# Performance work log

Hardware: AMD Instinct MI355X
Metric: run time of the kernel (lower is better)

The kernel has to match this reference:

```python
import jax, jax.numpy as jnp
import numpy as np

N_NODES = 50000
N_EDGES = 800000
N_GRAPHS = 64


def graph_conv(x, edge_index, w_rel, b_rel, w_root):
    # PyG GraphConv with aggr='add':
    #   out = lin_rel(sum_{j in N(i)} x_j) + lin_root(x_i)
    src, dst = edge_index[0], edge_index[1]
    agg = jax.ops.segment_sum(x[src], dst, num_segments=x.shape[0])  # [N, d_in]
    return agg @ w_rel + b_rel + x @ w_root  # [N, d_out]


def scatter_mean(x, batch, num_segments):
    s = jax.ops.segment_sum(x, batch, num_segments=num_segments)
    cnt = jax.ops.segment_sum(jnp.ones((x.shape[0],), x.dtype), batch,
                              num_segments=num_segments)
    return s / jnp.maximum(cnt, 1.0)[:, None]


def setup_inputs() -> dict:
    key = jax.random.key(0)
    ks = jax.random.split(key, 8)
    d_feat, d_hid, d_out = 128, 128, 128
    x = jax.random.normal(ks[0], (N_NODES, d_feat), dtype=jnp.float32)
    edge_index = jax.random.randint(ks[1], (2, N_EDGES), 0, N_NODES, dtype=jnp.int64)
    batch = jnp.sort(jax.random.randint(ks[2], (N_NODES,), 0, N_GRAPHS, dtype=jnp.int64))

    def glorot(k, shape):
        fan_in = shape[0]
        return jax.random.normal(k, shape, dtype=jnp.float32) / np.sqrt(fan_in)

    return {
        "x": x,
        "edge_index": edge_index,
        "batch": batch,
        "w_rel1": glorot(ks[3], (d_feat, d_hid)),
        "b_rel1": jnp.zeros((d_hid,), jnp.float32),
        "w_root1": glorot(ks[4], (d_feat, d_hid)),
        "w_rel2": glorot(ks[5], (d_hid, 2 * d_hid)),
        "b_rel2": jnp.zeros((2 * d_hid,), jnp.float32),
        "w_root2": glorot(ks[6], (d_hid, 2 * d_hid)),
        "w_rel3": glorot(ks[7], (2 * d_hid, d_out)),
        "b_rel3": jnp.zeros((d_out,), jnp.float32),
        "w_root3": glorot(jax.random.fold_in(key, 99), (2 * d_hid, d_out)),
    }


def reference(x, edge_index, batch,
              w_rel1, b_rel1, w_root1,
              w_rel2, b_rel2, w_root2,
              w_rel3, b_rel3, w_root3):
    h = jax.nn.elu(graph_conv(x, edge_index, w_rel1, b_rel1, w_root1))
    h = jax.nn.elu(graph_conv(h, edge_index, w_rel2, b_rel2, w_root2))
    h = jax.nn.elu(graph_conv(h, edge_index, w_rel3, b_rel3, w_root3))
    return scatter_mean(h, batch, N_GRAPHS)  # [num_graphs, n_out]
```

## Files before the change

kernel.cpp:

```cpp
#include <hip/hip_runtime.h>
#include <math.h>

#define NN 50000
#define NNP 50048
#define NE 800000
#define NG 64
#define NBK 196
#define ECH 4082
#define TOTH (NBK * NBK)
#define NBH 151
#define SBLK 6890
#define SWORK (NN * 32 + 163840)
#define AGB 12500

typedef __attribute__((ext_vector_type(8))) __bf16 bf16x8;
typedef __attribute__((ext_vector_type(4))) float f32x4;

__device__ inline unsigned short f2bf(float f) {
    unsigned int u = __float_as_uint(f);
    u += 0x7fffu + ((u >> 16) & 1u);
    return (unsigned short)(u >> 16);
}
__device__ inline float bflo(unsigned int v) { return __uint_as_float(v << 16); }
__device__ inline float bfhi(unsigned int v) { return __uint_as_float(v & 0xffff0000u); }
__device__ inline float bfs(unsigned short v) { return __uint_as_float((unsigned int)v << 16); }

#define GLD_LDS16(g, l)                                                          \
    __builtin_amdgcn_global_load_lds(                                            \
        (const __attribute__((address_space(1))) unsigned int*)(g),              \
        (__attribute__((address_space(3))) unsigned int*)(l), 16, 0, 0)

__global__ __launch_bounds__(256) void front_k(const float* __restrict__ x,
                                               const float* __restrict__ wr1,
                                               const float* __restrict__ wo1,
                                               const float* __restrict__ wr2,
                                               const float* __restrict__ wo2,
                                               const float* __restrict__ wr3,
                                               const float* __restrict__ wo3,
                                               const int* __restrict__ edst,
                                               const int* __restrict__ batch,
                                               unsigned short* __restrict__ xb,
                                               unsigned short* __restrict__ W1T,
                                               unsigned short* __restrict__ W2T,
                                               unsigned short* __restrict__ W3T,
                                               int* __restrict__ H,
                                               int* __restrict__ bounds,
                                               float* __restrict__ outp) {
    const int b = blockIdx.x, t = threadIdx.x;
    if (b < SBLK) {
        int id = b * 256 + t;
        if (id < NN * 32) {
            float4 v = ((const float4*)x)[id];
            unsigned int p0 = ((unsigned int)f2bf(v.y) << 16) | f2bf(v.x);
            unsigned int p1 = ((unsigned int)f2bf(v.w) << 16) | f2bf(v.z);
            ((uint2*)xb)[id] = make_uint2(p0, p1);
            return;
        }
        int w = id - NN * 32;
        if (w < 32768) {
            int n = w >> 8, k = w & 255;
            W1T[w] = f2bf((k < 128) ? wr1[k * 128 + n] : wo1[(k - 128) * 128 + n]);
        } else if (w < 98304) {
            int j = w - 32768; int n = j >> 8, k = j & 255;
            W2T[j] = f2bf((k < 128) ? wr2[k * 256 + n] : wo2[(k - 128) * 256 + n]);
        } else if (w < 163840) {
            int j = w - 98304; int n = j >> 8, k = j & 255;
            W3T[j] = f2bf((n < 128) ? wr3[k * 128 + n] : wo3[k * 128 + (n - 128)]);
        }
        return;
    }
    if (b < SBLK + NBK) {
        __shared__ int h[NBK];
        int k = b - SBLK;
        if (t < NBK) h[t] = 0;
        __syncthreads();
        int e0 = k * ECH, e1 = min(NE, e0 + ECH);
        for (int e = e0 + t; e < e1; e += 256) atomicAdd(&h[edst[e] >> 8], 1);
        __syncthreads();
        if (t < NBK) H[t * NBK + k] = h[t];
        return;
    }
    if (t <= NG) {
        int g = t, lo = 0, hi = NN;
        while (lo < hi) { int mid = (lo + hi) >> 1; if (batch[mid] < g) lo = mid + 1; else hi = mid; }
        bounds[g] = lo;
    }
    for (int i = t; i < NG * 128; i += 256) outp[i] = 0.f;
}

__global__ __launch_bounds__(256) void hsum_k(const int* __restrict__ H,
                                              int* __restrict__ hb) {
    int i = blockIdx.x * 256 + threadIdx.x;
    int v = (i < TOTH) ? H[i] : 0;
    for (int off = 32; off; off >>= 1) v += __shfl_xor(v, off, 64);
    __shared__ int ws[4];
    if ((threadIdx.x & 63) == 0) ws[threadIdx.x >> 6] = v;
    __syncthreads();
    if (threadIdx.x == 0) hb[blockIdx.x] = ws[0] + ws[1] + ws[2] + ws[3];
}

__global__ __launch_bounds__(256) void happly_k(const int* __restrict__ H,
                                                const int* __restrict__ hb,
                                                int* __restrict__ S) {
    __shared__ int s[256], ws[4], choff;
    const int t = threadIdx.x, c = blockIdx.x;
    {
        int v = (t < c) ? hb[t] : 0;
        for (int off = 32; off; off >>= 1) v += __shfl_xor(v, off, 64);
        if ((t & 63) == 0) ws[t >> 6] = v;
        __syncthreads();
        if (t == 0) choff = ws[0] + ws[1] + ws[2] + ws[3];
        __syncthreads();
    }
    int i = c * 256 + t;
    int v = (i < TOTH) ? H[i] : 0;
    s[t] = v; __syncthreads();
    for (int off = 1; off < 256; off <<= 1) {
        int u = (t >= off) ? s[t - off] : 0;
        __syncthreads(); s[t] += u; __syncthreads();
    }
    if (i < TOTH) S[i] = choff + s[t] - v;
}

__global__ __launch_bounds__(256) void scatter_k(const int* __restrict__ src,
                                                 const int* __restrict__ dst,
                                                 const int* __restrict__ S,
                                                 int* __restrict__ tmp) {
    __shared__ int cur[NBK];
    int t = threadIdx.x, k = blockIdx.x;
    if (t < NBK) cur[t] = S[t * NBK + k];
    __syncthreads();
    int e0 = k * ECH, e1 = min(NE, e0 + ECH);
    for (int e = e0 + t; e < e1; e += 256) {
        int d = dst[e];
        int p = atomicAdd(&cur[d >> 8], 1);
        tmp[p] = ((d & 255) << 16) | src[e];
    }
}

__global__ __launch_bounds__(256) void csr_k(const int* __restrict__ tmp,
                                             const int* __restrict__ S,
                                             int* __restrict__ rowptr,
                                             int* __restrict__ colsrc) {
    __shared__ int hist[256], off[256], cur[256];
    int t = threadIdx.x, b = blockIdx.x;
    int base = S[b * NBK];
    int next = (b < NBK - 1) ? S[(b + 1) * NBK] : NE;
    int cntb = next - base;
    hist[t] = 0;
    __syncthreads();
    for (int i = t; i < cntb; i += 256) atomicAdd(&hist[tmp[base + i] >> 16], 1);
    __syncthreads();
    int v = hist[t];
    off[t] = v; __syncthreads();
    for (int o = 1; o < 256; o <<= 1) {
        int u = (t >= o) ? off[t - o] : 0;
        __syncthreads(); off[t] += u; __syncthreads();
    }
    int excl = off[t] - v;
    int node = b * 256 + t;
    if (node <= NN) rowptr[node] = base + excl;
    cur[t] = excl;
    __syncthreads();
    for (int i = t; i < cntb; i += 256) {
        int e = tmp[base + i];
        int p = atomicAdd(&cur[e >> 16], 1);
        colsrc[base + p] = e & 0xffff;
    }
}

__global__ __launch_bounds__(256) void aggs_k(const unsigned short* __restrict__ feat,
                                              const int* __restrict__ rowptr,
                                              const int* __restrict__ colsrc,
                                              unsigned short* __restrict__ outp) {
    const int slice = blockIdx.x & 3;
    const int gid = threadIdx.x >> 4;
    const int l16 = threadIdx.x & 15;
    const int node = (blockIdx.x >> 2) * 16 + gid;
    const int fo = slice * 32 + l16 * 2;
    const int beg = rowptr[node], end = rowptr[node + 1];
    float ax = 0.f, ay = 0.f;
    int e = beg;
    for (; e + 8 <= end; e += 8) {
        int c[8];
#pragma unroll
        for (int i = 0; i < 8; ++i) c[i] = colsrc[e + i];
        unsigned int v[8];
#pragma unroll
        for (int i = 0; i < 8; ++i)
            v[i] = *(const unsigned int*)&feat[(size_t)c[i] * 128 + fo];
#pragma unroll
        for (int i = 0; i < 8; ++i) { ax += bflo(v[i]); ay += bfhi(v[i]); }
    }
    for (; e < end; ++e) {
        unsigned int v = *(const unsigned int*)&feat[(size_t)colsrc[e] * 128 + fo];
        ax += bflo(v); ay += bfhi(v);
    }
    unsigned int p = ((unsigned int)f2bf(ay) << 16) | f2bf(ax);
    *(unsigned int*)&outp[(size_t)node * 128 + fo] = p;
}

__global__ __launch_bounds__(256) void aggfs_k(const unsigned short* __restrict__ y,
                                               const unsigned short* __restrict__ rr,
                                               const float* __restrict__ b3,
                                               const int* __restrict__ rowptr,
                                               const int* __restrict__ colsrc,
                                               unsigned short* __restrict__ outp) {
    const int slice = blockIdx.x & 3;
    const int gid = threadIdx.x >> 4;
    const int l16 = threadIdx.x & 15;
    const int node = (blockIdx.x >> 2) * 16 + gid;
    const int fo = slice * 32 + l16 * 2;
    const int beg = rowptr[node], end = rowptr[node + 1];
    float ax = 0.f, ay = 0.f;
    int e = beg;
    for (; e + 8 <= end; e += 8) {
        int c[8];
#pragma unroll
        for (int i = 0; i < 8; ++i) c[i] = colsrc[e + i];
        unsigned int v[8];
#pragma unroll
        for (int i = 0; i < 8; ++i)
            v[i] = *(const unsigned int*)&y[(size_t)c[i] * 128 + fo];
#pragma unroll
        for (int i = 0; i < 8; ++i) { ax += bflo(v[i]); ay += bfhi(v[i]); }
    }
    for (; e < end; ++e) {
        unsigned int v = *(const unsigned int*)&y[(size_t)colsrc[e] * 128 + fo];
        ax += bflo(v); ay += bfhi(v);
    }
    unsigned int rv = *(const unsigned int*)&rr[(size_t)node * 128 + fo];
    float2 bb = *(const float2*)&b3[fo];
    float vx = ax + bflo(rv) + bb.x;
    float vy = ay + bfhi(rv) + bb.y;
    vx = vx > 0.f ? vx : (__expf(vx) - 1.f);
    vy = vy > 0.f ? vy : (__expf(vy) - 1.f);
    unsigned int p = ((unsigned int)f2bf(vy) << 16) | f2bf(vx);
    *(unsigned int*)&outp[(size_t)node * 128 + fo] = p;
}

template <int MT, int KA, int N, bool TWO, bool BIAS, bool ELU>
__global__ __launch_bounds__(256) void gemm_k(const unsigned short* __restrict__ A1,
                                              const unsigned short* __restrict__ A2,
                                              const unsigned short* __restrict__ WT,
                                              const float* __restrict__ bias,
                                              unsigned short* __restrict__ Cout) {
    constexpr int KTOT = TWO ? 2 * KA : KA;
    constexpr int NSTEP = KTOT / 32;
    constexpr int MI = MT / 32;
    constexpr int LA = MT / 64;
    constexpr int LB = N / 64;
    __shared__ __attribute__((aligned(16))) unsigned short As[2][MT * 32];
    __shared__ __attribute__((aligned(16))) unsigned short Bs[2][N * 32];
    const int t = threadIdx.x;
    const int wv = t >> 6, lane = t & 63;
    const int qd = lane >> 4, l16 = lane & 15;
    const int m0 = blockIdx.x * MT;
    const int mh = (wv & 1) * (MT / 2), nh = (wv >> 1) * 64;
    const int srow = lane >> 2;
    const int skk  = (lane & 3) * 8;

    f32x4 acc[MI][4] = {};

    auto stage = [&](int k0, int buf) {
        const unsigned short* Abase = (TWO && k0 >= KA) ? (A2 + (k0 - KA)) : (A1 + k0);
#pragma unroll
        for (int i = 0; i < LA; ++i) {
            int chunk = wv * LA + i;
            const unsigned short* g = Abase + (size_t)(m0 + chunk * 16 + srow) * KA + skk;
            GLD_LDS16(g, &As[buf][chunk * 512]);
        }
        const unsigned short* Wbase = WT + k0;
#pragma unroll
        for (int i = 0; i < LB; ++i) {
            int chunk = wv * LB + i;
            const unsigned short* g = Wbase + (size_t)(chunk * 16 + srow) * KTOT + skk;
            GLD_LDS16(g, &Bs[buf][chunk * 512]);
        }
    };

    stage(0, 0);
    for (int s = 0; s < NSTEP; ++s) {
        const int cur = s & 1;
        if (s + 1 < NSTEP) {
            stage((s + 1) * 32, cur ^ 1);
            asm volatile("s_waitcnt vmcnt(%0)" :: "i"(LA + LB) : "memory");
        } else {
            asm volatile("s_waitcnt vmcnt(0)" ::: "memory");
        }
        __builtin_amdgcn_s_barrier();
        asm volatile("" ::: "memory");
        bf16x8 af[MI], bfr[4];
#pragma unroll
        for (int mi = 0; mi < MI; ++mi)
            af[mi] = *(const bf16x8*)&As[cur][(mh + mi * 16 + l16) * 32 + qd * 8];
#pragma unroll
        for (int ni = 0; ni < 4; ++ni)
            bfr[ni] = *(const bf16x8*)&Bs[cur][(nh + ni * 16 + l16) * 32 + qd * 8];
#pragma unroll
        for (int mi = 0; mi < MI; ++mi)
#pragma unroll
            for (int ni = 0; ni < 4; ++ni)
                acc[mi][ni] = __builtin_amdgcn_mfma_f32_16x16x32_bf16(
                    af[mi], bfr[ni], acc[mi][ni], 0, 0, 0);
        asm volatile("" ::: "memory");
        __builtin_amdgcn_s_barrier();
    }

#pragma unroll
    for (int mi = 0; mi < MI; ++mi)
#pragma unroll
        for (int ni = 0; ni < 4; ++ni)
#pragma unroll
            for (int r = 0; r < 4; ++r) {
                int mm = m0 + mh + mi * 16 + qd * 4 + r;
                if (mm < NN) {
                    int nn = nh + ni * 16 + l16;
                    float v = acc[mi][ni][r];
                    if (BIAS) v += bias[nn];
                    if (ELU) v = v > 0.f ? v : (__expf(v) - 1.f);
                    Cout[(size_t)mm * N + nn] = f2bf(v);
                }
            }
}

template <int KA, bool TWO, bool BIAS, bool ELU, bool SPLIT>
__global__ __launch_bounds__(256) void gemm256_k(const unsigned short* __restrict__ A1,
                                                 const unsigned short* __restrict__ A2,
                                                 const unsigned short* __restrict__ WT,
                                                 const float* __restrict__ bias,
                                                 unsigned short* __restrict__ Cout,
                                                 unsigned short* __restrict__ Cout2) {
    constexpr int KTOT = TWO ? 2 * KA : KA;
    constexpr int NSTEP = KTOT / 32;
    __shared__ __attribute__((aligned(16))) unsigned short As[2][64 * 32];
    __shared__ __attribute__((aligned(16))) unsigned short Bs[2][256 * 32];
    const int t = threadIdx.x;
    const int wv = t >> 6, lane = t & 63;
    const int qd = lane >> 4, l16 = lane & 15;
    const int m0 = blockIdx.x * 64;
    const int srow = lane >> 2;
    const int skk  = (lane & 3) * 8;

    f32x4 acc[4][4] = {};

    auto stage = [&](int k0, int buf) {
        const unsigned short* Abase = (TWO && k0 >= KA) ? (A2 + (k0 - KA)) : (A1 + k0);
        {
            const unsigned short* g = Abase + (size_t)(m0 + wv * 16 + srow) * KA + skk;
            GLD_LDS16(g, &As[buf][wv * 512]);
        }
        const unsigned short* Wbase = WT + k0;
#pragma unroll
        for (int i = 0; i < 4; ++i) {
            int chunk = wv * 4 + i;
            const unsigned short* g = Wbase + (size_t)(chunk * 16 + srow) * KTOT + skk;
            GLD_LDS16(g, &Bs[buf][chunk * 512]);
        }
    };

    stage(0, 0);
    for (int s = 0; s < NSTEP; ++s) {
        const int cur = s & 1;
        if (s + 1 < NSTEP) {
            stage((s + 1) * 32, cur ^ 1);
            asm volatile("s_waitcnt vmcnt(%0)" :: "i"(5) : "memory");
        } else {
            asm volatile("s_waitcnt vmcnt(0)" ::: "memory");
        }
        __builtin_amdgcn_s_barrier();
        asm volatile("" ::: "memory");
        bf16x8 af[4], bfr[4];
#pragma unroll
        for (int mi = 0; mi < 4; ++mi)
            af[mi] = *(const bf16x8*)&As[cur][(mi * 16 + l16) * 32 + qd * 8];
#pragma unroll
        for (int ni = 0; ni < 4; ++ni)
            bfr[ni] = *(const bf16x8*)&Bs[cur][(wv * 64 + ni * 16 + l16) * 32 + qd * 8];
#pragma unroll
        for (int mi = 0; mi < 4; ++mi)
#pragma unroll
            for (int ni = 0; ni < 4; ++ni)
                acc[mi][ni] = __builtin_amdgcn_mfma_f32_16x16x32_bf16(
                    af[mi], bfr[ni], acc[mi][ni], 0, 0, 0);
        asm volatile("" ::: "memory");
        __builtin_amdgcn_s_barrier();
    }

#pragma unroll
    for (int mi = 0; mi < 4; ++mi)
#pragma unroll
        for (int ni = 0; ni < 4; ++ni)
#pragma unroll
            for (int r = 0; r < 4; ++r) {
                int mm = m0 + mi * 16 + qd * 4 + r;
                if (mm < NN) {
                    int nn = wv * 64 + ni * 16 + l16;
                    float v = acc[mi][ni][r];
                    if (BIAS) v += bias[nn];
                    if (ELU) v = v > 0.f ? v : (__expf(v) - 1.f);
                    unsigned short b = f2bf(v);
                    if (SPLIT) {
                        unsigned short* dst = (nn < 128) ? Cout : Cout2;
                        dst[(size_t)mm * 128 + (nn & 127)] = b;
                    } else {
                        Cout[(size_t)mm * 256 + nn] = b;
                    }
                }
            }
}

__global__ __launch_bounds__(256) void sum_k(const unsigned short* __restrict__ vals,
                                             const int* __restrict__ batch,
                                             float* __restrict__ outsum) {
    const int CH = 25;
    int wv = threadIdx.x >> 6, lane = threadIdx.x & 63;
    int n0 = (blockIdx.x * 4 + wv) * CH;
    int g = batch[n0];
    float ax = 0.f, ay = 0.f;
    for (int i = 0; i < CH; ++i) {
        int n = n0 + i;
        int gn = batch[n];
        if (gn != g) {
            unsafeAtomicAdd(&outsum[(size_t)g * 128 + lane * 2], ax);
            unsafeAtomicAdd(&outsum[(size_t)g * 128 + lane * 2 + 1], ay);
            ax = 0.f; ay = 0.f; g = gn;
        }
        unsigned int v = *(const unsigned int*)&vals[(size_t)n * 128 + lane * 2];
        ax += bflo(v); ay += bfhi(v);
    }
    unsafeAtomicAdd(&outsum[(size_t)g * 128 + lane * 2], ax);
    unsafeAtomicAdd(&outsum[(size_t)g * 128 + lane * 2 + 1], ay);
}

__global__ void divide_k(const int* __restrict__ bounds, float* __restrict__ out) {
    int i = blockIdx.x * 256 + threadIdx.x;
    if (i < NG * 128) {
        int g = i >> 7;
        float c = (float)(bounds[g + 1] - bounds[g]);
        out[i] /= fmaxf(c, 1.f);
    }
}

extern "C" void kernel_launch(void* const* d_in, const int* in_sizes, int n_in,
                              void* d_out, int out_size, void* d_ws, size_t ws_size,
                              hipStream_t stream) {
    const float* x       = (const float*)d_in[0];
    const int*   ei      = (const int*)d_in[1];
    const int*   batch   = (const int*)d_in[2];
    const float* w_rel1  = (const float*)d_in[3];
    const float* b_rel1  = (const float*)d_in[4];
    const float* w_root1 = (const float*)d_in[5];
    const float* w_rel2  = (const float*)d_in[6];
    const float* b_rel2  = (const float*)d_in[7];
    const float* w_root2 = (const float*)d_in[8];
    const float* w_rel3  = (const float*)d_in[9];
    const float* b_rel3  = (const float*)d_in[10];
    const float* w_root3 = (const float*)d_in[11];
    const int* esrc = ei;
    const int* edst = ei + NE;

    unsigned short* Ab = (unsigned short*)d_ws;
    unsigned short* Bb = Ab + (size_t)NNP * 128;
    unsigned short* Cb = Bb + (size_t)NNP * 128;
    unsigned short* xb = Cb + (size_t)NNP * 256;
    unsigned short* W1T = xb + (size_t)NNP * 128;
    unsigned short* W2T = W1T + 128 * 256;
    unsigned short* W3T = W2T + 256 * 256;
    int* rowptr = (int*)(W3T + 256 * 256);
    int* colsrc = rowptr + (NN + 1);
    int* tmp    = colsrc + NE;
    int* H      = tmp + NE;
    int* S      = H + TOTH;
    int* hb     = S + TOTH;
    int* bounds = hb + 256;
    float* outp = (float*)d_out;

    front_k<<<SBLK + NBK + 1, 256, 0, stream>>>(
        x, w_rel1, w_root1, w_rel2, w_root2, w_rel3, w_root3, edst, batch,
        xb, W1T, W2T, W3T, H, bounds, outp);
    hsum_k<<<NBH, 256, 0, stream>>>(H, hb);
    happly_k<<<NBH, 256, 0, stream>>>(H, hb, S);
    scatter_k<<<NBK, 256, 0, stream>>>(esrc, edst, S, tmp);
    csr_k<<<NBK, 256, 0, stream>>>(tmp, S, rowptr, colsrc);

    aggs_k<<<AGB, 256, 0, stream>>>(xb, rowptr, colsrc, Ab);
    gemm_k<64, 128, 128, true, true, true>
        <<<NNP / 64, 256, 0, stream>>>(Ab, xb, W1T, b_rel1, Bb);

    aggs_k<<<AGB, 256, 0, stream>>>(Bb, rowptr, colsrc, Ab);
    gemm256_k<128, true, true, true, false>
        <<<NNP / 64, 256, 0, stream>>>(Ab, Bb, W2T, b_rel2, Cb, nullptr);

    gemm256_k<256, false, false, false, true>
        <<<NNP / 64, 256, 0, stream>>>(Cb, nullptr, W3T, nullptr, Ab, Bb);

    aggfs_k<<<AGB, 256, 0, stream>>>(Ab, Bb, b_rel3, rowptr, colsrc, Cb);
    sum_k<<<NN / 100, 256, 0, stream>>>(Cb, batch, outp);
    divide_k<<<(NG * 128 + 255) / 256, 256, 0, stream>>>(bounds, outp);
}
```

Measured before the change: 362.9 us.

## Assign one wavefront per node in CSR aggregation with split edge halves

The three gather-aggregation kernels now map one 64-lane wavefront to each destination node instead of 16 lanes per node per 32-feature slice. Each half-wave handles alternate edges with 8-byte loads covering the full 128-feature row, and the halves are combined with a cross-lane shuffle before the bf16 store. This cuts redundant rowptr and colsrc reads, which were repeated by four slice blocks, and widens the per-lane loads. In exchange, half the lanes sit idle during the epilogue and store, and there is extra tail-handling code.

```diff
diff --git a/kernel.cpp b/kernel.cpp
--- a/kernel.cpp
+++ b/kernel.cpp
@@ -11,7 +11,6 @@
 #define NBH 151
 #define SBLK 6890
 #define SWORK (NN * 32 + 163840)
-#define AGB 12500
 
 typedef __attribute__((ext_vector_type(8))) __bf16 bf16x8;
 typedef __attribute__((ext_vector_type(4))) float f32x4;
@@ -169,74 +168,132 @@
     }
 }
 
-__global__ __launch_bounds__(256) void aggs_k(const unsigned short* __restrict__ feat,
+__global__ __launch_bounds__(256) void aggb_k(const unsigned short* __restrict__ feat,
                                               const int* __restrict__ rowptr,
                                               const int* __restrict__ colsrc,
                                               unsigned short* __restrict__ outp) {
-    const int slice = blockIdx.x & 3;
-    const int gid = threadIdx.x >> 4;
-    const int l16 = threadIdx.x & 15;
-    const int node = (blockIdx.x >> 2) * 16 + gid;
-    const int fo = slice * 32 + l16 * 2;
+    const int node = __builtin_amdgcn_readfirstlane((int)(blockIdx.x * 4 + (threadIdx.x >> 6)));
+    const int lane = threadIdx.x & 63;
+    const int half = lane >> 5, l32 = lane & 31;
     const int beg = rowptr[node], end = rowptr[node + 1];
-    float ax = 0.f, ay = 0.f;
+    float a0 = 0.f, a1 = 0.f, a2 = 0.f, a3 = 0.f;
     int e = beg;
-    for (; e + 8 <= end; e += 8) {
-        int c[8];
-#pragma unroll
-        for (int i = 0; i < 8; ++i) c[i] = colsrc[e + i];
-        unsigned int v[8];
+    for (; e + 16 <= end; e += 16) {
+        int c[8]; uint2 v[8];
+#pragma unroll
+        for (int i = 0; i < 8; ++i) c[i] = colsrc[e + 2 * i + half];
 #pragma unroll
         for (int i = 0; i < 8; ++i)
-            v[i] = *(const unsigned int*)&feat[(size_t)c[i] * 128 + fo];
-#pragma unroll
-        for (int i = 0; i < 8; ++i) { ax += bflo(v[i]); ay += bfhi(v[i]); }
-    }
-    for (; e < end; ++e) {
-        unsigned int v = *(const unsigned int*)&feat[(size_t)colsrc[e] * 128 + fo];
-        ax += bflo(v); ay += bfhi(v);
-    }
-    unsigned int p = ((unsigned int)f2bf(ay) << 16) | f2bf(ax);
-    *(unsigned int*)&outp[(size_t)node * 128 + fo] = p;
-}
-
-__global__ __launch_bounds__(256) void aggfs_k(const unsigned short* __restrict__ y,
-                                               const unsigned short* __restrict__ rr,
-                                               const float* __restrict__ b3,
-                                               const int* __restrict__ rowptr,
-                                               const int* __restrict__ colsrc,
-                                               unsigned short* __restrict__ outp) {
-    const int slice = blockIdx.x & 3;
-    const int gid = threadIdx.x >> 4;
-    const int l16 = threadIdx.x & 15;
-    const int node = (blockIdx.x >> 2) * 16 + gid;
-    const int fo = slice * 32 + l16 * 2;
+            v[i] = *(const uint2*)&feat[(size_t)c[i] * 128 + l32 * 4];
+#pragma unroll
+        for (int i = 0; i < 8; ++i) {
+            a0 += bflo(v[i].x); a1 += bfhi(v[i].x);
+            a2 += bflo(v[i].y); a3 += bfhi(v[i].y);
+        }
+    }
+    for (; e + 4 <= end; e += 4) {
+        int c[2]; uint2 v[2];
+#pragma unroll
+        for (int i = 0; i < 2; ++i) c[i] = colsrc[e + 2 * i + half];
+#pragma unroll
+        for (int i = 0; i < 2; ++i)
+            v[i] = *(const uint2*)&feat[(size_t)c[i] * 128 + l32 * 4];
+#pragma unroll
+        for (int i = 0; i < 2; ++i) {
+            a0 += bflo(v[i].x); a1 += bfhi(v[i].x);
+            a2 += bflo(v[i].y); a3 += bfhi(v[i].y);
+        }
+    }
+    if (e + 2 <= end) {
+        int c = colsrc[e + half];
+        uint2 v = *(const uint2*)&feat[(size_t)c * 128 + l32 * 4];
+        a0 += bflo(v.x); a1 += bfhi(v.x); a2 += bflo(v.y); a3 += bfhi(v.y);
+        e += 2;
+    }
+    if (e < end && half == 0) {
+        int c = colsrc[e];
+        uint2 v = *(const uint2*)&feat[(size_t)c * 128 + l32 * 4];
+        a0 += bflo(v.x); a1 += bfhi(v.x); a2 += bflo(v.y); a3 += bfhi(v.y);
+    }
+    a0 += __shfl_xor(a0, 32, 64);
+    a1 += __shfl_xor(a1, 32, 64);
+    a2 += __shfl_xor(a2, 32, 64);
+    a3 += __shfl_xor(a3, 32, 64);
+    if (half == 0) {
+        unsigned int p0 = ((unsigned int)f2bf(a1) << 16) | f2bf(a0);
+        unsigned int p1 = ((unsigned int)f2bf(a3) << 16) | f2bf(a2);
+        *(uint2*)&outp[(size_t)node * 128 + l32 * 4] = make_uint2(p0, p1);
+    }
+}
+
+__global__ __launch_bounds__(256) void aggf_k(const unsigned short* __restrict__ y,
+                                              const unsigned short* __restrict__ rr,
+                                              const float* __restrict__ b3,
+                                              const int* __restrict__ rowptr,
+                                              const int* __restrict__ colsrc,
+                                              unsigned short* __restrict__ outp) {
+    const int node = __builtin_amdgcn_readfirstlane((int)(blockIdx.x * 4 + (threadIdx.x >> 6)));
+    const int lane = threadIdx.x & 63;
+    const int half = lane >> 5, l32 = lane & 31;
     const int beg = rowptr[node], end = rowptr[node + 1];
-    float ax = 0.f, ay = 0.f;
+    float a0 = 0.f, a1 = 0.f, a2 = 0.f, a3 = 0.f;
     int e = beg;
-    for (; e + 8 <= end; e += 8) {
-        int c[8];
-#pragma unroll
-        for (int i = 0; i < 8; ++i) c[i] = colsrc[e + i];
-        unsigned int v[8];
+    for (; e + 16 <= end; e += 16) {
+        int c[8]; uint2 v[8];
+#pragma unroll
+        for (int i = 0; i < 8; ++i) c[i] = colsrc[e + 2 * i + half];
 #pragma unroll
         for (int i = 0; i < 8; ++i)
-            v[i] = *(const unsigned int*)&y[(size_t)c[i] * 128 + fo];
-#pragma unroll
-        for (int i = 0; i < 8; ++i) { ax += bflo(v[i]); ay += bfhi(v[i]); }
-    }
-    for (; e < end; ++e) {
-        unsigned int v = *(const unsigned int*)&y[(size_t)colsrc[e] * 128 + fo];
-        ax += bflo(v); ay += bfhi(v);
-    }
-    unsigned int rv = *(const unsigned int*)&rr[(size_t)node * 128 + fo];
-    float2 bb = *(const float2*)&b3[fo];
-    float vx = ax + bflo(rv) + bb.x;
-    float vy = ay + bfhi(rv) + bb.y;
-    vx = vx > 0.f ? vx : (__expf(vx) - 1.f);
-    vy = vy > 0.f ? vy : (__expf(vy) - 1.f);
-    unsigned int p = ((unsigned int)f2bf(vy) << 16) | f2bf(vx);
-    *(unsigned int*)&outp[(size_t)node * 128 + fo] = p;
+            v[i] = *(const uint2*)&y[(size_t)c[i] * 128 + l32 * 4];
+#pragma unroll
+        for (int i = 0; i < 8; ++i) {
+            a0 += bflo(v[i].x); a1 += bfhi(v[i].x);
+            a2 += bflo(v[i].y); a3 += bfhi(v[i].y);
+        }
+    }
+    for (; e + 4 <= end; e += 4) {
+        int c[2]; uint2 v[2];
+#pragma unroll
+        for (int i = 0; i < 2; ++i) c[i] = colsrc[e + 2 * i + half];
+#pragma unroll
+        for (int i = 0; i < 2; ++i)
+            v[i] = *(const uint2*)&y[(size_t)c[i] * 128 + l32 * 4];
+#pragma unroll
+        for (int i = 0; i < 2; ++i) {
+            a0 += bflo(v[i].x); a1 += bfhi(v[i].x);
+            a2 += bflo(v[i].y); a3 += bfhi(v[i].y);
+        }
+    }
+    if (e + 2 <= end) {
+        int c = colsrc[e + half];
+        uint2 v = *(const uint2*)&y[(size_t)c * 128 + l32 * 4];
+        a0 += bflo(v.x); a1 += bfhi(v.x); a2 += bflo(v.y); a3 += bfhi(v.y);
+        e += 2;
+    }
+    if (e < end && half == 0) {
+        int c = colsrc[e];
+        uint2 v = *(const uint2*)&y[(size_t)c * 128 + l32 * 4];
+        a0 += bflo(v.x); a1 += bfhi(v.x); a2 += bflo(v.y); a3 += bfhi(v.y);
+    }
+    a0 += __shfl_xor(a0, 32, 64);
+    a1 += __shfl_xor(a1, 32, 64);
+    a2 += __shfl_xor(a2, 32, 64);
+    a3 += __shfl_xor(a3, 32, 64);
+    if (half == 0) {
+        uint2 rv = *(const uint2*)&rr[(size_t)node * 128 + l32 * 4];
+        float4 bb = *(const float4*)&b3[l32 * 4];
+        float v0 = a0 + bflo(rv.x) + bb.x;
+        float v1 = a1 + bfhi(rv.x) + bb.y;
+        float v2 = a2 + bflo(rv.y) + bb.z;
+        float v3 = a3 + bfhi(rv.y) + bb.w;
+        v0 = v0 > 0.f ? v0 : (__expf(v0) - 1.f);
+        v1 = v1 > 0.f ? v1 : (__expf(v1) - 1.f);
+        v2 = v2 > 0.f ? v2 : (__expf(v2) - 1.f);
+        v3 = v3 > 0.f ? v3 : (__expf(v3) - 1.f);
+        unsigned int p0 = ((unsigned int)f2bf(v1) << 16) | f2bf(v0);
+        unsigned int p1 = ((unsigned int)f2bf(v3) << 16) | f2bf(v2);
+        *(uint2*)&outp[(size_t)node * 128 + l32 * 4] = make_uint2(p0, p1);
+    }
 }
 
 template <int MT, int KA, int N, bool TWO, bool BIAS, bool ELU>
@@ -484,18 +541,18 @@
     scatter_k<<<NBK, 256, 0, stream>>>(esrc, edst, S, tmp);
     csr_k<<<NBK, 256, 0, stream>>>(tmp, S, rowptr, colsrc);
 
-    aggs_k<<<AGB, 256, 0, stream>>>(xb, rowptr, colsrc, Ab);
+    aggb_k<<<NN / 4, 256, 0, stream>>>(xb, rowptr, colsrc, Ab);
     gemm_k<64, 128, 128, true, true, true>
         <<<NNP / 64, 256, 0, stream>>>(Ab, xb, W1T, b_rel1, Bb);
 
-    aggs_k<<<AGB, 256, 0, stream>>>(Bb, rowptr, colsrc, Ab);
+    aggb_k<<<NN / 4, 256, 0, stream>>>(Bb, rowptr, colsrc, Ab);
     gemm256_k<128, true, true, true, false>
         <<<NNP / 64, 256, 0, stream>>>(Ab, Bb, W2T, b_rel2, Cb, nullptr);
 
     gemm256_k<256, false, false, false, true>
         <<<NNP / 64, 256, 0, stream>>>(Cb, nullptr, W3T, nullptr, Ab, Bb);
 
-    aggfs_k<<<AGB, 256, 0, stream>>>(Ab, Bb, b_rel3, rowptr, colsrc, Cb);
+    aggf_k<<<NN / 4, 256, 0, stream>>>(Ab, Bb, b_rel3, rowptr, colsrc, Cb);
     sum_k<<<NN / 100, 256, 0, stream>>>(Cb, batch, outp);
     divide_k<<<(NG * 128 + 255) / 256, 256, 0, stream>>>(bounds, outp);
 }
```

Measured after the change: 299.4 us. 17.5% less time.
